# Performance work log

Measured on AMD Instinct MI355X. Metric: run time of the kernel, lower is better.

Reference implementation:

```python
import jax, jax.numpy as jnp
import numpy as np

N = 100_000   # nodes
E = 3_200_000 # edges (avg degree 32)
EPS = 1e-5


def setup_inputs() -> dict:
    key = jax.random.key(0)
    ks = jax.random.split(key, 20)

    def w(k, i, o):
        return jax.random.normal(k, (i, o), jnp.float32) / np.float32(np.sqrt(i))

    return {
        "x": jax.random.normal(ks[0], (N, 5), jnp.float32),
        "src": jax.random.randint(ks[1], (E,), 0, N),
        "dst": jax.random.randint(ks[2], (E,), 0, N),
        "W1": w(ks[3], 5, 64),  "b1": jnp.zeros((64,), jnp.float32),
        "g1": jnp.ones((64,), jnp.float32), "be1": jnp.zeros((64,), jnp.float32),
        "m1": jax.random.normal(ks[4], (64,), jnp.float32) * 0.1,
        "v1": jax.random.uniform(ks[5], (64,), jnp.float32, 0.5, 1.5),
        "W2": w(ks[6], 64, 32), "b2": jnp.zeros((32,), jnp.float32),
        "g2": jnp.ones((32,), jnp.float32), "be2": jnp.zeros((32,), jnp.float32),
        "m2": jax.random.normal(ks[7], (32,), jnp.float32) * 0.1,
        "v2": jax.random.uniform(ks[8], (32,), jnp.float32, 0.5, 1.5),
        "W3": w(ks[9], 32, 16), "b3": jnp.zeros((16,), jnp.float32),
        "W4": w(ks[10], 16, 3), "b4": jnp.zeros((3,), jnp.float32),
    }


def _gcn_conv(h, W, b, src, dst, dinv):
    # PyG GCNConv: add self-loops, symmetric deg^-1/2 normalization,
    # linear transform, scatter-add aggregation, bias.
    h = h @ W                                    # [N, out]
    norm = dinv[src] * dinv[dst]                 # [E]
    agg = jax.ops.segment_sum(norm[:, None] * h[src], dst, num_segments=N)
    agg = agg + (dinv * dinv)[:, None] * h       # self-loop term
    return agg + b


def _bn(x, g, be, m, v):
    # BatchNorm1d in eval mode (running stats)
    return (x - m) * jax.lax.rsqrt(v + EPS) * g + be


def reference(x, src, dst,
              W1, b1, g1, be1, m1, v1,
              W2, b2, g2, be2, m2, v2,
              W3, b3, W4, b4):
    # degree including self-loops (edge weights = 1)
    deg = jax.ops.segment_sum(jnp.ones((E,), x.dtype), dst, num_segments=N) + 1.0
    dinv = jax.lax.rsqrt(deg)

    h = jax.nn.relu(_bn(_gcn_conv(x, W1, b1, src, dst, dinv), g1, be1, m1, v1))
    # dropout p=0.15: identity in eval mode
    h = jax.nn.relu(_bn(_gcn_conv(h, W2, b2, src, dst, dinv), g2, be2, m2, v2))
    # dropout p=0.10: identity in eval mode
    h = jax.nn.relu(_gcn_conv(h, W3, b3, src, dst, dinv))
    return _gcn_conv(h, W4, b4, src, dst, dinv)   # [N, 3] logits
```

## Files before the change

### kernel.cpp

```cpp
#include <hip/hip_runtime.h>
#include <hip/hip_fp16.h>

static constexpr int NN = 100000;
static constexpr int NE = 3200000;
static constexpr float EPS = 1e-5f;
static constexpr int NB   = 391;
static constexpr int CAP2 = 9216;
static constexpr int CH1  = 4096;
static constexpr int NBLK1 = (NE + CH1 - 1) / CH1;

typedef _Float16 h2f __attribute__((ext_vector_type(2)));

__device__ __forceinline__ h2f u2h2(unsigned u) {
    union { unsigned u; h2f h; } cv; cv.u = u; return cv.h;
}

__global__ void k_seed(int* __restrict__ gcur) {
    int t = blockIdx.x * blockDim.x + threadIdx.x;
    if (t < NB) gcur[t] = t * CAP2;
}

__global__ __launch_bounds__(512) void k_part1(const int* __restrict__ src,
                                               const int* __restrict__ dst,
                                               int* __restrict__ gcur,
                                               unsigned* __restrict__ ebuf) {
    __shared__ unsigned stage[CH1];
    __shared__ unsigned short bins[CH1];
    __shared__ int hist[NB], lbase[NB + 1], lcur[NB], gbase[NB];
    int tid = threadIdx.x;
    int e0 = blockIdx.x * CH1;
    int n = min(CH1, NE - e0);

    for (int t = tid; t < NB; t += 512) { hist[t] = 0; lcur[t] = 0; }
    __syncthreads();
    for (int i = tid; i < n; i += 512) atomicAdd(&hist[dst[e0 + i] >> 8], 1);
    __syncthreads();
    for (int t = tid; t < NB; t += 512) gbase[t] = atomicAdd(&gcur[t], hist[t]);
    if (tid < 64) {
        int lane = tid, sum = 0, pre[7];
        #pragma unroll
        for (int k = 0; k < 7; ++k) {
            int idx = lane * 7 + k;
            int v = (idx < NB) ? hist[idx] : 0;
            pre[k] = sum; sum += v;
        }
        int inc = sum;
        #pragma unroll
        for (int off = 1; off < 64; off <<= 1) {
            int t = __shfl_up(inc, off);
            if (lane >= off) inc += t;
        }
        int excl = inc - sum;
        #pragma unroll
        for (int k = 0; k < 7; ++k) {
            int idx = lane * 7 + k;
            if (idx < NB + 1) lbase[idx] = excl + pre[k];
        }
    }
    __syncthreads();
    for (int i = tid; i < n; i += 512) {
        int d = dst[e0 + i];
        int b = d >> 8;
        int r = atomicAdd(&lcur[b], 1);
        int p = lbase[b] + r;
        stage[p] = ((unsigned)(d & 255) << 17) | (unsigned)src[e0 + i];
        bins[p] = (unsigned short)b;
    }
    __syncthreads();
    for (int i = tid; i < n; i += 512) {
        int b = bins[i];
        ebuf[gbase[b] + (i - lbase[b])] = stage[i];
    }
}

__global__ void k_binscan(const int* __restrict__ gcur, int* __restrict__ binBase) {
    __shared__ int s[512];
    int t = threadIdx.x;
    int v = (t < NB) ? (gcur[t] - t * CAP2) : 0;
    s[t] = v;
    __syncthreads();
    for (int off = 1; off < 512; off <<= 1) {
        int x = (t >= off) ? s[t - off] : 0;
        __syncthreads();
        s[t] += x;
        __syncthreads();
    }
    if (t < NB + 1) binBase[t] = s[t] - v;
}

__global__ __launch_bounds__(512) void k_part2(const unsigned* __restrict__ ebuf,
                                               const int* __restrict__ binBase,
                                               int* __restrict__ csr, int* __restrict__ rowp,
                                               int* __restrict__ cnt, float* __restrict__ dinv,
                                               const float* __restrict__ x,
                                               float* __restrict__ q) {
    __shared__ unsigned s2[CAP2];
    __shared__ int lhist[256], lrow[257];
    __shared__ float ldinv[256];
    int tid = threadIdx.x, b = blockIdx.x;
    int base = b * CAP2;
    int o0 = binBase[b], m = binBase[b + 1] - o0;

    if (tid < 256) lhist[tid] = 0;
    __syncthreads();
    for (int i = tid; i < m; i += 512) atomicAdd(&lhist[ebuf[base + i] >> 17], 1);
    __syncthreads();
    if (tid < 64) {
        int lane = tid, sum = 0, pre[4];
        #pragma unroll
        for (int k = 0; k < 4; ++k) { pre[k] = sum; sum += lhist[lane * 4 + k]; }
        int inc = sum;
        #pragma unroll
        for (int off = 1; off < 64; off <<= 1) {
            int t = __shfl_up(inc, off);
            if (lane >= off) inc += t;
        }
        int excl = inc - sum;
        #pragma unroll
        for (int k = 0; k < 4; ++k) lrow[lane * 4 + k] = excl + pre[k];
        if (lane == 63) lrow[256] = excl + sum;
    }
    __syncthreads();
    if (tid < 256) lhist[tid] = 0;
    __syncthreads();
    for (int i = tid; i < m; i += 512) {
        unsigned p = ebuf[base + i];
        int nd = (int)(p >> 17);
        int r = atomicAdd(&lhist[nd], 1);
        s2[lrow[nd] + r] = p & 0x1FFFFu;
    }
    __syncthreads();
    for (int i = tid; i < m; i += 512) csr[o0 + i] = (int)s2[i];
    int ng = (b << 8) + tid;
    if (tid < 256 && ng < NN) {
        int c = lrow[tid + 1] - lrow[tid];
        rowp[ng] = o0 + lrow[tid];
        cnt[ng] = c;
        float dv = rsqrtf((float)c + 1.f);
        dinv[ng] = dv;
        ldinv[tid] = dv;
    }
    __syncthreads();
    int nmax = min(256, NN - (b << 8));
    for (int idx = tid; idx < nmax * 8; idx += 512) {
        int nl = idx >> 3, k = idx & 7;
        int node = (b << 8) + nl;
        q[(size_t)node * 8 + k] = (k < 5) ? x[node * 5 + k] * ldinv[nl] : 0.f;
    }
}

template<int INP, int IN, int OUT, int OUTP, int MODE>
__global__ __launch_bounds__(256) void k_lin(
        const float* __restrict__ in, const float* __restrict__ W,
        const float* __restrict__ dinv, const float* __restrict__ b,
        const float* __restrict__ g, const float* __restrict__ be,
        const float* __restrict__ m, const float* __restrict__ vv,
        float* __restrict__ outf, __half* __restrict__ outh) {
    constexpr int NPB = 256 / OUTP;
    __shared__ float srow[NPB * INP];
    __shared__ float sW[IN * OUT];
    int tid = threadIdx.x;
    size_t node0 = (size_t)blockIdx.x * NPB;

    for (int t = tid; t < IN * OUT; t += 256) sW[t] = W[t];
    const float4* in4 = reinterpret_cast<const float4*>(in + node0 * INP);
    float4* s4 = reinterpret_cast<float4*>(srow);
    constexpr int TOT4 = NPB * INP / 4;
    #pragma unroll 1
    for (int t = tid; t < TOT4; t += 256) s4[t] = in4[t];
    __syncthreads();

    int il = tid / OUTP, f = tid - il * OUTP;
    size_t node = node0 + il;
    if (node >= NN) return;
    const float* row = srow + il * INP;
    float a = 0.f;
    if (f < OUT) {
        #pragma unroll
        for (int k = 0; k < IN; ++k) a += row[k] * sW[k * OUT + f];
    }
    if constexpr (MODE == 0) {
        outf[node * OUTP + f] = (f < OUT) ? a * dinv[node] : 0.f;
    } else if constexpr (MODE == 1) {
        outh[node * OUT + f] = __float2half(a * dinv[node]);
    } else {
        float z = a + b[f];
        z = (z - m[f]) * rsqrtf(vv[f] + EPS) * g[f] + be[f];
        outf[node * OUT + f] = fmaxf(z, 0.f);
    }
}

template<int F, int MODE>
__global__ __launch_bounds__(256) void k_gather(
        const int* __restrict__ row_ptr, const int* __restrict__ cnt,
        const int* __restrict__ csr, const float* __restrict__ hs,
        const float* __restrict__ dinv, const float* __restrict__ b,
        float* __restrict__ out) {
    constexpr int F4   = F / 4;
    constexpr int EPI  = 32 / F4;
    constexpr int ITER = F4;

    int wid  = (blockIdx.x * blockDim.x + threadIdx.x) >> 6;
    int lane = threadIdx.x & 63;
    int half = lane >> 5, hl = lane & 31;
    int node = wid * 2 + half;
    if (node >= NN) return;
    int c = hl & (F4 - 1);
    int e = hl / F4;

    int start = row_ptr[node];
    int n     = cnt[node];

    float4 a = make_float4(0.f, 0.f, 0.f, 0.f);
    for (int base = 0; base < n; base += 32) {
        int rem = n - base;
        int my = (hl < rem) ? csr[start + base + hl] : 0;
        #pragma unroll
        for (int k = 0; k < ITER; ++k) {
            if (k * EPI >= rem) break;
            int j = e + k * EPI;
            int t = __shfl(my, half * 32 + j);
            bool act = (j < rem);
            int s = act ? t : 0;
            float4 v = reinterpret_cast<const float4*>(hs + (size_t)s * F)[c];
            if (act) { a.x += v.x; a.y += v.y; a.z += v.z; a.w += v.w; }
        }
    }
    #pragma unroll
    for (int mask = F4; mask < 32; mask <<= 1) {
        a.x += __shfl_xor(a.x, mask);
        a.y += __shfl_xor(a.y, mask);
        a.z += __shfl_xor(a.z, mask);
        a.w += __shfl_xor(a.w, mask);
    }

    if (hl < F4) {
        float4 self = reinterpret_cast<const float4*>(hs + (size_t)node * F)[hl];
        float di = dinv[node];
        float4 z;
        z.x = di * (a.x + self.x);
        z.y = di * (a.y + self.y);
        z.z = di * (a.z + self.z);
        z.w = di * (a.w + self.w);
        if constexpr (MODE == 3) {
            float* o = out + (size_t)node * 3;
            o[0] = z.x + b[0]; o[1] = z.y + b[1]; o[2] = z.z + b[2];
        } else {
            reinterpret_cast<float4*>(out + (size_t)node * F)[hl] = z;
        }
    }
}

template<int F, int MODE>
__global__ __launch_bounds__(256) void k_gather_h(
        const int* __restrict__ row_ptr, const int* __restrict__ cnt,
        const int* __restrict__ csr, const __half* __restrict__ hs,
        const float* __restrict__ dinv, const float* __restrict__ b,
        const float* __restrict__ g, const float* __restrict__ be,
        const float* __restrict__ m, const float* __restrict__ vv,
        float* __restrict__ out) {
    constexpr int F4   = F / 4;
    constexpr int EPI  = 32 / F4;
    constexpr int ITER = F4;

    int wid  = (blockIdx.x * blockDim.x + threadIdx.x) >> 6;
    int lane = threadIdx.x & 63;
    int half = lane >> 5, hl = lane & 31;
    int node = wid * 2 + half;
    if (node >= NN) return;
    int c = hl & (F4 - 1);
    int e = hl / F4;

    int start = row_ptr[node];
    int n     = cnt[node];

    const h2f SEL_A = {(_Float16)1.f, (_Float16)0.f};
    const h2f SEL_B = {(_Float16)0.f, (_Float16)1.f};
    const h2f SEL_Z = {(_Float16)0.f, (_Float16)0.f};

    float4 a = make_float4(0.f, 0.f, 0.f, 0.f);
    for (int base = 0; base < n; base += 32) {
        int rem = n - base;
        int my = (hl < rem) ? csr[start + base + hl] : 0;
        #pragma unroll
        for (int k = 0; k < ITER; ++k) {
            if (k * EPI >= rem) break;
            int j = e + k * EPI;
            int t = __shfl(my, half * 32 + j);
            bool act = (j < rem);
            int s = act ? t : 0;
            uint2 r = reinterpret_cast<const uint2*>(hs + (size_t)s * F)[c];
            h2f sA = act ? SEL_A : SEL_Z;
            h2f sB = act ? SEL_B : SEL_Z;
            h2f h0 = u2h2(r.x), h1 = u2h2(r.y);
            a.x = __builtin_amdgcn_fdot2(h0, sA, a.x, false);
            a.y = __builtin_amdgcn_fdot2(h0, sB, a.y, false);
            a.z = __builtin_amdgcn_fdot2(h1, sA, a.z, false);
            a.w = __builtin_amdgcn_fdot2(h1, sB, a.w, false);
        }
    }
    #pragma unroll
    for (int mask = F4; mask < 32; mask <<= 1) {
        a.x += __shfl_xor(a.x, mask);
        a.y += __shfl_xor(a.y, mask);
        a.z += __shfl_xor(a.z, mask);
        a.w += __shfl_xor(a.w, mask);
    }

    if (hl < F4) {
        uint2 r = reinterpret_cast<const uint2*>(hs + (size_t)node * F)[hl];
        float2 s0 = __half22float2(*reinterpret_cast<__half2*>(&r.x));
        float2 s1 = __half22float2(*reinterpret_cast<__half2*>(&r.y));
        float di = dinv[node];
        int f0 = hl * 4;
        float4 z;
        z.x = di * (a.x + s0.x) + b[f0 + 0];
        z.y = di * (a.y + s0.y) + b[f0 + 1];
        z.z = di * (a.z + s1.x) + b[f0 + 2];
        z.w = di * (a.w + s1.y) + b[f0 + 3];
        if constexpr (MODE == 2) {
            z.x = (z.x - m[f0+0]) * rsqrtf(vv[f0+0] + EPS) * g[f0+0] + be[f0+0];
            z.y = (z.y - m[f0+1]) * rsqrtf(vv[f0+1] + EPS) * g[f0+1] + be[f0+1];
            z.z = (z.z - m[f0+2]) * rsqrtf(vv[f0+2] + EPS) * g[f0+2] + be[f0+2];
            z.w = (z.w - m[f0+3]) * rsqrtf(vv[f0+3] + EPS) * g[f0+3] + be[f0+3];
        }
        z.x = fmaxf(z.x, 0.f); z.y = fmaxf(z.y, 0.f);
        z.z = fmaxf(z.z, 0.f); z.w = fmaxf(z.w, 0.f);
        reinterpret_cast<float4*>(out + (size_t)node * F)[hl] = z;
    }
}

extern "C" void kernel_launch(void* const* d_in, const int* in_sizes, int n_in,
                              void* d_out, int out_size, void* d_ws, size_t ws_size,
                              hipStream_t stream) {
    const float* x   = (const float*)d_in[0];
    const int*   src = (const int*)  d_in[1];
    const int*   dst = (const int*)  d_in[2];
    const float* W1  = (const float*)d_in[3];
    const float* b1  = (const float*)d_in[4];
    const float* g1  = (const float*)d_in[5];
    const float* be1 = (const float*)d_in[6];
    const float* m1  = (const float*)d_in[7];
    const float* v1  = (const float*)d_in[8];
    const float* W2  = (const float*)d_in[9];
    const float* b2  = (const float*)d_in[10];
    const float* g2  = (const float*)d_in[11];
    const float* be2 = (const float*)d_in[12];
    const float* m2  = (const float*)d_in[13];
    const float* v2  = (const float*)d_in[14];
    const float* W3  = (const float*)d_in[15];
    const float* b3  = (const float*)d_in[16];
    const float* W4  = (const float*)d_in[17];
    const float* b4  = (const float*)d_in[18];
    float* out = (float*)d_out;

    char* wsb = (char*)d_ws;
    float*    dinv    = (float*)wsb;
    int*      cnt     = (int*)(wsb + 100352ull * 4);
    int*      rowp    = (int*)(wsb + 200704ull * 4);
    int*      gcur    = (int*)(wsb + 301056ull * 4);
    int*      binBase = (int*)(wsb + 301568ull * 4);
    int*      csr     = (int*)(wsb + 302080ull * 4);
    float*    HS      = (float*)(wsb + (302080ull + NE) * 4);
    __half*   HSh     = (__half*)HS;
    float*    X       = (float*)(wsb + (302080ull + NE + 6400000ull) * 4);
    unsigned* ebuf    = (unsigned*)X;
    float*    G       = (float*)(wsb + (302080ull + NE + 12800000ull) * 4);

    const int BLK = 256;
    const int gW2 = ((NN + 1) / 2 * 64 + BLK - 1) / BLK;

    k_seed   <<<2, 256, 0, stream>>>(gcur);
    k_part1  <<<NBLK1, 512, 0, stream>>>(src, dst, gcur, ebuf);
    k_binscan<<<1, 512, 0, stream>>>(gcur, binBase);
    k_part2  <<<NB, 512, 0, stream>>>(ebuf, binBase, csr, rowp, cnt, dinv, x, HS);

    k_gather<8, 0><<<gW2, BLK, 0, stream>>>(rowp, cnt, csr, HS, dinv, nullptr, G);
    k_lin<8, 5, 64, 64, 2><<<(NN + 3) / 4, BLK, 0, stream>>>(
        G, W1, nullptr, b1, g1, be1, m1, v1, X, nullptr);

    k_lin<64, 64, 32, 32, 1><<<(NN + 7) / 8, BLK, 0, stream>>>(
        X, W2, dinv, nullptr, nullptr, nullptr, nullptr, nullptr, nullptr, HSh);
    k_gather_h<32, 2><<<gW2, BLK, 0, stream>>>(rowp, cnt, csr, HSh, dinv, b2, g2, be2, m2, v2, X);

    k_lin<32, 32, 16, 16, 1><<<(NN + 15) / 16, BLK, 0, stream>>>(
        X, W3, dinv, nullptr, nullptr, nullptr, nullptr, nullptr, nullptr, HSh);
    k_gather_h<16, 1><<<gW2, BLK, 0, stream>>>(rowp, cnt, csr, HSh, dinv, b3,
                                               nullptr, nullptr, nullptr, nullptr, X);

    k_lin<16, 16, 3, 4, 0><<<(NN + 63) / 64, BLK, 0, stream>>>(
        X, W4, dinv, nullptr, nullptr, nullptr, nullptr, nullptr, HS, nullptr);
    k_gather<4, 3><<<gW2, BLK, 0, stream>>>(rowp, cnt, csr, HS, dinv, b4, out);
}
```

Baseline: 237.6 us.

## Split layer-2 gather into two 16-column passes and use fp16 for layer-1 input

Layer 1's scaled input features are now stored in fp16 and aggregated with the half-precision gather kernel instead of the fp32 one. The layer-2 transform writes its 32-wide output as two column-blocked planes of 16 halves. The aggregation then runs as two separate 16-feature gathers, each writing its half of the output row through a new stride/offset parameter. This aims to shrink the per-pass gathered working set so random neighbour reads hit cache more often, at the cost of traversing the edge list twice and some fp16 precision loss on the input features.

```diff
diff --git a/kernel.cpp b/kernel.cpp
--- a/kernel.cpp
+++ b/kernel.cpp
@@ -93,7 +93,7 @@
                                                int* __restrict__ csr, int* __restrict__ rowp,
                                                int* __restrict__ cnt, float* __restrict__ dinv,
                                                const float* __restrict__ x,
-                                               float* __restrict__ q) {
+                                               __half* __restrict__ q) {
     __shared__ unsigned s2[CAP2];
     __shared__ int lhist[256], lrow[257];
     __shared__ float ldinv[256];
@@ -145,7 +145,7 @@
     for (int idx = tid; idx < nmax * 8; idx += 512) {
         int nl = idx >> 3, k = idx & 7;
         int node = (b << 8) + nl;
-        q[(size_t)node * 8 + k] = (k < 5) ? x[node * 5 + k] * ldinv[nl] : 0.f;
+        q[(size_t)node * 8 + k] = __float2half((k < 5) ? x[node * 5 + k] * ldinv[nl] : 0.f);
     }
 }
 
@@ -183,10 +183,12 @@
         outf[node * OUTP + f] = (f < OUT) ? a * dinv[node] : 0.f;
     } else if constexpr (MODE == 1) {
         outh[node * OUT + f] = __float2half(a * dinv[node]);
-    } else {
+    } else if constexpr (MODE == 2) {
         float z = a + b[f];
         z = (z - m[f]) * rsqrtf(vv[f] + EPS) * g[f] + be[f];
         outf[node * OUT + f] = fmaxf(z, 0.f);
+    } else {
+        outh[(size_t)(f >> 4) * NN * 16 + node * 16 + (f & 15)] = __float2half(a * dinv[node]);
     }
 }
 
@@ -251,14 +253,14 @@
     }
 }
 
-template<int F, int MODE>
+template<int F, int MODE, int OSTRIDE>
 __global__ __launch_bounds__(256) void k_gather_h(
         const int* __restrict__ row_ptr, const int* __restrict__ cnt,
         const int* __restrict__ csr, const __half* __restrict__ hs,
         const float* __restrict__ dinv, const float* __restrict__ b,
         const float* __restrict__ g, const float* __restrict__ be,
         const float* __restrict__ m, const float* __restrict__ vv,
-        float* __restrict__ out) {
+        float* __restrict__ out, int colOff) {
     constexpr int F4   = F / 4;
     constexpr int EPI  = 32 / F4;
     constexpr int ITER = F4;
@@ -314,19 +316,23 @@
         float di = dinv[node];
         int f0 = hl * 4;
         float4 z;
-        z.x = di * (a.x + s0.x) + b[f0 + 0];
-        z.y = di * (a.y + s0.y) + b[f0 + 1];
-        z.z = di * (a.z + s1.x) + b[f0 + 2];
-        z.w = di * (a.w + s1.y) + b[f0 + 3];
-        if constexpr (MODE == 2) {
-            z.x = (z.x - m[f0+0]) * rsqrtf(vv[f0+0] + EPS) * g[f0+0] + be[f0+0];
-            z.y = (z.y - m[f0+1]) * rsqrtf(vv[f0+1] + EPS) * g[f0+1] + be[f0+1];
-            z.z = (z.z - m[f0+2]) * rsqrtf(vv[f0+2] + EPS) * g[f0+2] + be[f0+2];
-            z.w = (z.w - m[f0+3]) * rsqrtf(vv[f0+3] + EPS) * g[f0+3] + be[f0+3];
-        }
-        z.x = fmaxf(z.x, 0.f); z.y = fmaxf(z.y, 0.f);
-        z.z = fmaxf(z.z, 0.f); z.w = fmaxf(z.w, 0.f);
-        reinterpret_cast<float4*>(out + (size_t)node * F)[hl] = z;
+        z.x = di * (a.x + s0.x);
+        z.y = di * (a.y + s0.y);
+        z.z = di * (a.z + s1.x);
+        z.w = di * (a.w + s1.y);
+        if constexpr (MODE >= 1) {
+            z.x += b[f0 + 0]; z.y += b[f0 + 1];
+            z.z += b[f0 + 2]; z.w += b[f0 + 3];
+            if constexpr (MODE == 2) {
+                z.x = (z.x - m[f0+0]) * rsqrtf(vv[f0+0] + EPS) * g[f0+0] + be[f0+0];
+                z.y = (z.y - m[f0+1]) * rsqrtf(vv[f0+1] + EPS) * g[f0+1] + be[f0+1];
+                z.z = (z.z - m[f0+2]) * rsqrtf(vv[f0+2] + EPS) * g[f0+2] + be[f0+2];
+                z.w = (z.w - m[f0+3]) * rsqrtf(vv[f0+3] + EPS) * g[f0+3] + be[f0+3];
+            }
+            z.x = fmaxf(z.x, 0.f); z.y = fmaxf(z.y, 0.f);
+            z.z = fmaxf(z.z, 0.f); z.w = fmaxf(z.w, 0.f);
+        }
+        reinterpret_cast<float4*>(out + (size_t)node * OSTRIDE + colOff)[hl] = z;
     }
 }
 
@@ -373,20 +379,24 @@
     k_seed   <<<2, 256, 0, stream>>>(gcur);
     k_part1  <<<NBLK1, 512, 0, stream>>>(src, dst, gcur, ebuf);
     k_binscan<<<1, 512, 0, stream>>>(gcur, binBase);
-    k_part2  <<<NB, 512, 0, stream>>>(ebuf, binBase, csr, rowp, cnt, dinv, x, HS);
-
-    k_gather<8, 0><<<gW2, BLK, 0, stream>>>(rowp, cnt, csr, HS, dinv, nullptr, G);
+    k_part2  <<<NB, 512, 0, stream>>>(ebuf, binBase, csr, rowp, cnt, dinv, x, HSh);
+
+    k_gather_h<8, 0, 8><<<gW2, BLK, 0, stream>>>(rowp, cnt, csr, HSh, dinv,
+        nullptr, nullptr, nullptr, nullptr, nullptr, G, 0);
     k_lin<8, 5, 64, 64, 2><<<(NN + 3) / 4, BLK, 0, stream>>>(
         G, W1, nullptr, b1, g1, be1, m1, v1, X, nullptr);
 
-    k_lin<64, 64, 32, 32, 1><<<(NN + 7) / 8, BLK, 0, stream>>>(
+    k_lin<64, 64, 32, 32, 3><<<(NN + 7) / 8, BLK, 0, stream>>>(
         X, W2, dinv, nullptr, nullptr, nullptr, nullptr, nullptr, nullptr, HSh);
-    k_gather_h<32, 2><<<gW2, BLK, 0, stream>>>(rowp, cnt, csr, HSh, dinv, b2, g2, be2, m2, v2, X);
+    k_gather_h<16, 2, 32><<<gW2, BLK, 0, stream>>>(rowp, cnt, csr, HSh, dinv,
+        b2, g2, be2, m2, v2, X, 0);
+    k_gather_h<16, 2, 32><<<gW2, BLK, 0, stream>>>(rowp, cnt, csr, HSh + (size_t)NN * 16, dinv,
+        b2 + 16, g2 + 16, be2 + 16, m2 + 16, v2 + 16, X, 16);
 
     k_lin<32, 32, 16, 16, 1><<<(NN + 15) / 16, BLK, 0, stream>>>(
         X, W3, dinv, nullptr, nullptr, nullptr, nullptr, nullptr, nullptr, HSh);
-    k_gather_h<16, 1><<<gW2, BLK, 0, stream>>>(rowp, cnt, csr, HSh, dinv, b3,
-                                               nullptr, nullptr, nullptr, nullptr, X);
+    k_gather_h<16, 1, 16><<<gW2, BLK, 0, stream>>>(rowp, cnt, csr, HSh, dinv,
+        b3, nullptr, nullptr, nullptr, nullptr, X, 0);
 
     k_lin<16, 16, 3, 4, 0><<<(NN + 63) / 64, BLK, 0, stream>>>(
         X, W4, dinv, nullptr, nullptr, nullptr, nullptr, nullptr, HS, nullptr);
```

New measurement: 252.7 us. +6.3%, slower.
